# Kernel tuning notes

Hardware: AMD Instinct MI355X
Metric: run time of the kernel (lower is better)

## Reference

```python
import jax, jax.numpy as jnp
import numpy as np
from jax import lax

# Module hyperparameters (init_kwargs)
B, T, F, H = 512, 256, 64, 128
D = F + H            # decoder LSTMCell width = input_dim + hidden_rnn
OUT_DIM = 32         # output_dim (survival horizon steps)
RISKS = 2
NEG = -1e10


def lstm_cell(x, h, c, Wih, Whh):
    # PyTorch gate order: i, f, g, o; bias=False
    g = x @ Wih.T + h @ Whh.T
    i, f, gg, o = jnp.split(g, 4, axis=-1)
    c = jax.nn.sigmoid(f) * c + jax.nn.sigmoid(i) * jnp.tanh(gg)
    h = jax.nn.sigmoid(o) * jnp.tanh(c)
    return h, c


def setup_inputs() -> dict:
    key = jax.random.key(0)
    ks = jax.random.split(key, 12)
    rn = lambda k, shp, fan: jax.random.normal(k, shp, jnp.float32) * (1.0 / np.sqrt(fan))
    return {
        "x": jax.random.normal(ks[0], (B, T, F), jnp.float32),
        # encoder LSTM (1 layer, bias=False)
        "W_ih_emb": rn(ks[1], (4 * H, F), F),
        "W_hh_emb": rn(ks[2], (4 * H, H), H),
        # longitudinal head: Linear(H -> F)
        "W_long": rn(ks[3], (F, H), H),
        "b_long": jnp.zeros((F,), jnp.float32),
        # attention head: Linear(F+H -> 1)
        "W_att": rn(ks[4], (1, D), D),
        "b_att": jnp.zeros((1,), jnp.float32),
        # per-risk cause-specific LSTMCell (bias=False) and Linear(D -> 1)
        "W_ih_cs": rn(ks[5], (RISKS, 4 * D, D), D),
        "W_hh_cs": rn(ks[6], (RISKS, 4 * D, D), D),
        "W_cs": rn(ks[7], (RISKS, 1, D), D),
        "b_cs": jnp.zeros((RISKS, 1), jnp.float32),
    }


def _forward(x, W_ih_emb, W_hh_emb, W_long, b_long, W_att, b_att,
             W_ih_cs, W_hh_cs, W_cs, b_cs):
    inputmask = jnp.abs(x).sum(2) == 0                      # [B,T]
    last_obs = (~inputmask).sum(axis=1) - 1                 # [B]

    # encoder LSTM over time
    def enc_step(carry, xt):
        h, c = carry
        h, c = lstm_cell(xt, h, c, W_ih_emb, W_hh_emb)
        return (h, c), h

    h0 = jnp.zeros((x.shape[0], H), x.dtype)
    _, hs = lax.scan(enc_step, (h0, h0), x.transpose(1, 0, 2))
    hidden = hs.transpose(1, 0, 2)                          # [B,T,H]

    long_pred = hidden @ W_long.T + b_long                  # [B,T,F]

    x_last = x[jnp.arange(x.shape[0]), last_obs]            # [B,F]
    concat = jnp.concatenate(
        [hidden, jnp.broadcast_to(x_last[:, None, :], (x.shape[0], x.shape[1], F))], -1)
    scores = (concat @ W_att.T + b_att)[..., 0]             # [B,T]

    idx = jnp.arange(x.shape[1])[None, :]
    scores = jnp.where(idx >= last_obs[:, None], NEG, scores)
    att = jax.nn.softmax(scores, axis=1)
    att = jnp.where((last_obs > 0)[:, None], att, 0.0)      # rows with last_obs==0 zeroed

    hidden_att = jnp.einsum('bt,bth->bh', att, hidden)      # [B,H]
    ha = jnp.concatenate([hidden_att, x_last], 1)           # [B,D]

    state0 = (lax.stop_gradient(ha), lax.stop_gradient(ha))  # .detach() on init state
    rs = jnp.arange(OUT_DIM * RISKS) % RISKS                # k-major, r-minor loop order

    def dec_step(carry, r):
        h, c = carry
        h, c = lstm_cell(ha, h, c, W_ih_cs[r], W_hh_cs[r])
        out = jax.nn.sigmoid(h @ W_cs[r].T + b_cs[r])       # [B,1]
        return (h, c), out

    _, outs = lax.scan(dec_step, state0, rs)                # [steps,B,1]
    outcomes = jax.nn.softmax(outs[..., 0].T, axis=-1)      # [B, OUT_DIM*RISKS]
    parts = tuple(outcomes[:, i * OUT_DIM:(i + 1) * OUT_DIM] for i in range(RISKS))
    return (long_pred,) + parts


def reference(x, W_ih_emb, W_hh_emb, W_long, b_long, W_att, b_att,
              W_ih_cs, W_hh_cs, W_cs, b_cs):
    return _forward(x, W_ih_emb, W_hh_emb, W_long, b_long, W_att, b_att,
                    W_ih_cs, W_hh_cs, W_cs, b_cs)
```

## Files before the change

kernel.cpp:

```cpp
#include <hip/hip_runtime.h>
#include <stdint.h>

#define DEV __device__ __forceinline__
typedef unsigned short u16; typedef unsigned int u32; typedef unsigned long long u64;
typedef __attribute__((ext_vector_type(8))) short s8v;
typedef __attribute__((ext_vector_type(4))) float f4v;

#define Bb 512
#define Tt 256
#define Ff 64
#define Hh 128
#define Dd 192

DEV u16 f2bf(float f){ u32 u = __builtin_bit_cast(u32, f); u32 r = (u + 0x7fffu + ((u>>16)&1u)) >> 16; return (u16)r; }
DEV float bf2f(u16 h){ u32 u = ((u32)h)<<16; return __builtin_bit_cast(float, u); }
DEV float sigm(float x){ return __builtin_amdgcn_rcpf(1.0f + __expf(-x)); }
DEV float tanhfast(float x){ return 1.0f - 2.0f*__builtin_amdgcn_rcpf(1.0f + __expf(2.0f*x)); }

DEV f4v mfma16(s8v a, s8v b, f4v c){ return __builtin_amdgcn_mfma_f32_16x16x32_bf16(a, b, c, 0, 0, 0); }

DEV int hxe(int k, int c){ int blk = k>>3; return (blk*16 + (c ^ ((blk&3)<<1)))*8 + (k&7); }

DEV s8v pack8(const float* p){
  const float4 a = *(const float4*)p; const float4 b = *(const float4*)(p+4);
  s8v r; r[0]=(short)f2bf(a.x); r[1]=(short)f2bf(a.y); r[2]=(short)f2bf(a.z); r[3]=(short)f2bf(a.w);
  r[4]=(short)f2bf(b.x); r[5]=(short)f2bf(b.y); r[6]=(short)f2bf(b.z); r[7]=(short)f2bf(b.w); return r;
}

__global__ __launch_bounds__(64) void prelim_k(const float* __restrict__ x,
    const float* __restrict__ Watt, const float* __restrict__ batt,
    float* __restrict__ xlast, float* __restrict__ c0, int* __restrict__ lastobs)
{
  int b = blockIdx.x, tid = threadIdx.x;
  int cnt = 0;
  for (int it = 0; it < 4; ++it){
    int t = it*64 + tid;
    const float4* p = (const float4*)(x + ((size_t)b*Tt + t)*Ff);
    float s = 0.0f;
    #pragma unroll
    for (int q = 0; q < 16; ++q){ float4 v = p[q]; s += fabsf(v.x)+fabsf(v.y)+fabsf(v.z)+fabsf(v.w); }
    u64 m = __ballot(s != 0.0f);
    cnt += __popcll(m);
  }
  int last = cnt - 1;
  int li = (last < 0) ? (Tt-1) : last;
  float xl = x[((size_t)b*Tt + li)*Ff + tid];
  xlast[b*Ff + tid] = xl;
  float p = xl * Watt[Hh + tid];
  for (int off = 32; off; off >>= 1) p += __shfl_down(p, off);
  if (tid == 0){ c0[b] = p + batt[0]; lastobs[b] = last; }
}

__global__ __launch_bounds__(256) void prep_wd_k(const float* __restrict__ Whhcs, u16* __restrict__ Wd)
{
  int idx = blockIdx.x*256 + threadIdx.x;
  int j = idx & 7, l = (idx>>3)&63;
  int fidx = idx>>9;
  int kt = fidx % 6; int rem = fidx/6; int mt = rem & 3; rem >>= 2; int w = rem % 12; int r = rem/12;
  int gate = mt*Dd + w*16 + (l&15);
  int k = kt*32 + (l>>4)*8 + j;
  Wd[idx] = f2bf(Whhcs[((size_t)r*768 + gate)*Dd + k]);
}

__global__ __launch_bounds__(512) void enc_k(
    const float* __restrict__ x, const float* __restrict__ Whh, const float* __restrict__ Wih,
    const float* __restrict__ Wlong, const float* __restrict__ blong, const float* __restrict__ Watt,
    const float* __restrict__ xlast, const float* __restrict__ c0v, const int* __restrict__ lastobs,
    float* __restrict__ lp_out, float* __restrict__ ha)
{
  __shared__ __align__(16) u16 hx[3072];
  __shared__ float lp_lds[16*68];
  __shared__ float sarr[16];
  const int tid = threadIdx.x, wid = tid>>6, lane = tid&63, l15 = lane&15, l4 = lane>>4;
  const int b0 = blockIdx.x*16;
  const int xrow = tid>>5, xc2 = (tid&31)*2;

  s8v wf[4][6];
  #pragma unroll
  for (int mt = 0; mt < 4; ++mt){
    int gate = mt*Hh + wid*16 + l15;
    #pragma unroll
    for (int kt = 0; kt < 6; ++kt){
      int k0 = kt*32 + l4*8;
      if (kt < 4) wf[mt][kt] = pack8(Whh + (size_t)gate*Hh + k0);
      else        wf[mt][kt] = pack8(Wih + (size_t)gate*Ff + (k0 - Hh));
    }
  }
  s8v wfx[6];
  {
    s8v z = {0,0,0,0,0,0,0,0};
    #pragma unroll
    for (int kt = 0; kt < 6; ++kt) wfx[kt] = z;
    if (wid < 4){
      int f = wid*16 + l15;
      #pragma unroll
      for (int kt = 0; kt < 4; ++kt) wfx[kt] = pack8(Wlong + (size_t)f*Hh + kt*32 + l4*8);
    } else if (wid == 4 && l15 == 0){
      #pragma unroll
      for (int kt = 0; kt < 4; ++kt) wfx[kt] = pack8(Watt + kt*32 + l4*8);
    }
  }
  float bl[4] = {0,0,0,0};
  if (wid < 4){
    #pragma unroll
    for (int j = 0; j < 4; ++j) bl[j] = blong[wid*16 + l4*4 + j];
  }
  const int   lastb = lastobs[b0 + l15];
  const float c0b   = c0v[b0 + l15];

  ((u64*)hx)[tid] = 0ull;
  {
    float2 xv = *(const float2*)(x + ((size_t)(b0+xrow)*Tt + 0)*Ff + xc2);
    u32 pk = (u32)f2bf(xv.x) | ((u32)f2bf(xv.y)<<16);
    *(u32*)&hx[hxe(Hh + xc2, xrow)] = pk;
  }
  __syncthreads();

  float cst[4] = {0,0,0,0}, hval[4] = {0,0,0,0};
  float accA[4] = {0,0,0,0}, mrun = -3.0e38f, zrun = 0.0f;

  for (int t = 0; t < Tt; ++t){
    s8v bf[6];
    #pragma unroll
    for (int kt = 0; kt < 6; ++kt)
      bf[kt] = *(const s8v*)&hx[((kt*4 + l4)*16 + (l15 ^ (l4<<1)))*8];
    float2 xnext;
    if (t+1 < Tt) xnext = *(const float2*)(x + ((size_t)(b0+xrow)*Tt + (t+1))*Ff + xc2);

    f4v acc0 = {0,0,0,0}, acc1 = {0,0,0,0}, acc2 = {0,0,0,0}, acc3 = {0,0,0,0}, accx = {0,0,0,0};
    #pragma unroll
    for (int kt = 0; kt < 6; ++kt){
      acc0 = mfma16(wf[0][kt], bf[kt], acc0);
      acc1 = mfma16(wf[1][kt], bf[kt], acc1);
      acc2 = mfma16(wf[2][kt], bf[kt], acc2);
      acc3 = mfma16(wf[3][kt], bf[kt], acc3);
    }
    if (wid < 5){
      #pragma unroll
      for (int kt = 0; kt < 6; ++kt) accx = mfma16(wfx[kt], bf[kt], accx);
    }
    if (wid == 4 && l4 == 0) sarr[l15] = accx[0] + c0b;

    float hnew[4];
    #pragma unroll
    for (int j = 0; j < 4; ++j){
      float cn = sigm(acc1[j])*cst[j] + sigm(acc0[j])*tanhfast(acc2[j]);
      cst[j] = cn;
      hnew[j] = sigm(acc3[j])*tanhfast(cn);
    }
    __syncthreads();
    if (t >= 1){
      float s = sarr[l15];
      if (t-1 < lastb){
        float mn = fmaxf(mrun, s);
        float sc = __expf(mrun - mn);
        float e  = __expf(s - mn);
        zrun = zrun*sc + e;
        #pragma unroll
        for (int j = 0; j < 4; ++j) accA[j] = accA[j]*sc + e*hval[j];
        mrun = mn;
      }
    }
    #pragma unroll
    for (int j = 0; j < 4; ++j) hval[j] = hnew[j];
    #pragma unroll
    for (int j = 0; j < 4; ++j) hx[hxe(wid*16 + l4*4 + j, l15)] = (u16)f2bf(hnew[j]);
    if (t+1 < Tt){
      u32 pk = (u32)f2bf(xnext.x) | ((u32)f2bf(xnext.y)<<16);
      *(u32*)&hx[hxe(Hh + xc2, xrow)] = pk;
    }
    if (wid < 4){
      #pragma unroll
      for (int j = 0; j < 4; ++j)
        lp_lds[l15*68 + wid*16 + l4*4 + j] = accx[j] + bl[j];
    }
    __syncthreads();
    if (t >= 1){
      float2 v; v.x = lp_lds[xrow*68 + xc2]; v.y = lp_lds[xrow*68 + xc2 + 1];
      *(float2*)(lp_out + ((size_t)(b0+xrow)*Tt + (t-1))*Ff + xc2) = v;
    }
  }
  {
    s8v bf[4];
    #pragma unroll
    for (int kt = 0; kt < 4; ++kt)
      bf[kt] = *(const s8v*)&hx[((kt*4 + l4)*16 + (l15 ^ (l4<<1)))*8];
    if (wid < 4){
      f4v accx = {0,0,0,0};
      #pragma unroll
      for (int kt = 0; kt < 4; ++kt) accx = mfma16(wfx[kt], bf[kt], accx);
      #pragma unroll
      for (int j = 0; j < 4; ++j) lp_lds[l15*68 + wid*16 + l4*4 + j] = accx[j] + bl[j];
    }
    float inv = (zrun > 0.0f) ? __builtin_amdgcn_rcpf(zrun) : 0.0f;
    #pragma unroll
    for (int j = 0; j < 4; ++j)
      ha[(size_t)(b0 + l15)*Dd + wid*16 + l4*4 + j] = accA[j]*inv;
    __syncthreads();
    { float2 v; v.x = lp_lds[xrow*68 + xc2]; v.y = lp_lds[xrow*68 + xc2 + 1];
      *(float2*)(lp_out + ((size_t)(b0+xrow)*Tt + (Tt-1))*Ff + xc2) = v; }
    for (int q = tid; q < 16*Ff; q += 512){
      int r2 = q >> 6, f = q & 63;
      ha[(size_t)(b0 + r2)*Dd + Hh + f] = xlast[(b0 + r2)*Ff + f];
    }
  }
}

__global__ __launch_bounds__(768) void dec_k(const float* __restrict__ ha, const u16* __restrict__ Wd,
    const float* __restrict__ Wihcs, const float* __restrict__ Wcs, const float* __restrict__ bcs,
    float* __restrict__ outs)
{
  __shared__ __align__(16) u16 hx[3072];
  __shared__ float red[16*52];
  const int tid = threadIdx.x, wid = tid>>6, lane = tid&63, l15 = lane&15, l4 = lane>>4;
  const int b0 = blockIdx.x*16;
  {
    int k4 = tid>>4, c = tid&15, k = k4*4;
    float4 v = *(const float4*)(ha + (size_t)(b0+c)*Dd + k);
    int e = hxe(k, c);
    *(u32*)&hx[e]   = (u32)f2bf(v.x) | ((u32)f2bf(v.y)<<16);
    *(u32*)&hx[e+2] = (u32)f2bf(v.z) | ((u32)f2bf(v.w)<<16);
  }
  const int u0 = wid*16 + l4*4;
  float cst[4], wcs0[4], wcs1[4];
  #pragma unroll
  for (int j = 0; j < 4; ++j){
    cst[j]  = ha[(size_t)(b0+l15)*Dd + u0 + j];
    wcs0[j] = Wcs[u0 + j];
    wcs1[j] = Wcs[Dd + u0 + j];
  }
  const float bc0 = bcs[0], bc1 = bcs[1];
  __syncthreads();
  f4v xw0[4], xw1[4];
  {
    s8v haf[6];
    #pragma unroll
    for (int kt = 0; kt < 6; ++kt)
      haf[kt] = *(const s8v*)&hx[((kt*4 + l4)*16 + (l15 ^ (l4<<1)))*8];
    #pragma unroll
    for (int r = 0; r < 2; ++r)
      #pragma unroll
      for (int mt = 0; mt < 4; ++mt){
        f4v a = {0,0,0,0};
        #pragma unroll
        for (int kt = 0; kt < 6; ++kt){
          int gate = mt*Dd + wid*16 + l15;
          s8v w = pack8(Wihcs + ((size_t)r*768 + gate)*Dd + kt*32 + l4*8);
          a = mfma16(w, haf[kt], a);
        }
        if (r == 0) xw0[mt] = a; else xw1[mt] = a;
      }
  }
  for (int s = 0; s < 64; ++s){
    const int r = s & 1;
    s8v bf[6];
    #pragma unroll
    for (int kt = 0; kt < 6; ++kt)
      bf[kt] = *(const s8v*)&hx[((kt*4 + l4)*16 + (l15 ^ (l4<<1)))*8];
    const u16* wb = Wd + ((size_t)(r*12 + wid)*24)*512 + lane*8;
    f4v acc[4];
    s8v w0[6], w1[6];
    #pragma unroll
    for (int kt = 0; kt < 6; ++kt) w0[kt] = *(const s8v*)(wb + kt*512);
    {
      #pragma unroll
      for (int kt = 0; kt < 6; ++kt) w1[kt] = *(const s8v*)(wb + (6 + kt)*512);
      f4v a = r ? xw1[0] : xw0[0];
      #pragma unroll
      for (int kt = 0; kt < 6; ++kt) a = mfma16(w0[kt], bf[kt], a);
      acc[0] = a;
    }
    {
      #pragma unroll
      for (int kt = 0; kt < 6; ++kt) w0[kt] = *(const s8v*)(wb + (12 + kt)*512);
      f4v a = r ? xw1[1] : xw0[1];
      #pragma unroll
      for (int kt = 0; kt < 6; ++kt) a = mfma16(w1[kt], bf[kt], a);
      acc[1] = a;
    }
    {
      #pragma unroll
      for (int kt = 0; kt < 6; ++kt) w1[kt] = *(const s8v*)(wb + (18 + kt)*512);
      f4v a = r ? xw1[2] : xw0[2];
      #pragma unroll
      for (int kt = 0; kt < 6; ++kt) a = mfma16(w0[kt], bf[kt], a);
      acc[2] = a;
    }
    {
      f4v a = r ? xw1[3] : xw0[3];
      #pragma unroll
      for (int kt = 0; kt < 6; ++kt) a = mfma16(w1[kt], bf[kt], a);
      acc[3] = a;
    }
    float hnew[4], part = 0.0f;
    #pragma unroll
    for (int j = 0; j < 4; ++j){
      float cn = sigm(acc[1][j])*cst[j] + sigm(acc[0][j])*tanhfast(acc[2][j]);
      cst[j] = cn;
      hnew[j] = sigm(acc[3][j])*tanhfast(cn);
      part += hnew[j] * (r ? wcs1[j] : wcs0[j]);
    }
    __syncthreads();
    #pragma unroll
    for (int j = 0; j < 4; ++j) hx[hxe(u0 + j, l15)] = (u16)f2bf(hnew[j]);
    red[l15*52 + wid*4 + l4] = part;
    __syncthreads();
    if (tid < 16){
      float ssum = 0.0f;
      #pragma unroll
      for (int q = 0; q < 48; ++q) ssum += red[tid*52 + q];
      outs[s*Bb + b0 + tid] = sigm(ssum + (r ? bc1 : bc0));
    }
  }
}

__global__ __launch_bounds__(256) void fin_k(const float* __restrict__ outs, float* __restrict__ dout)
{
  int row = blockIdx.x*256 + threadIdx.x;
  float v[64]; float mx = -3.0e38f;
  #pragma unroll
  for (int s = 0; s < 64; ++s){ v[s] = outs[s*Bb + row]; mx = fmaxf(mx, v[s]); }
  float sum = 0.0f;
  #pragma unroll
  for (int s = 0; s < 64; ++s){ v[s] = __expf(v[s] - mx); sum += v[s]; }
  float inv = __builtin_amdgcn_rcpf(sum);
  float* p0 = dout + (size_t)Bb*Tt*Ff;
  float* p1 = p0 + Bb*32;
  #pragma unroll
  for (int j = 0; j < 32; ++j) p0[row*32 + j] = v[j]*inv;
  #pragma unroll
  for (int j = 0; j < 32; ++j) p1[row*32 + j] = v[32 + j]*inv;
}

extern "C" void kernel_launch(void* const* d_in, const int* in_sizes, int n_in,
                              void* d_out, int out_size, void* d_ws, size_t ws_size,
                              hipStream_t stream)
{
  const float* x      = (const float*)d_in[0];
  const float* Wih    = (const float*)d_in[1];
  const float* Whh    = (const float*)d_in[2];
  const float* Wlong  = (const float*)d_in[3];
  const float* blong  = (const float*)d_in[4];
  const float* Watt   = (const float*)d_in[5];
  const float* batt   = (const float*)d_in[6];
  const float* Wihcs  = (const float*)d_in[7];
  const float* Whhcs  = (const float*)d_in[8];
  const float* Wcs    = (const float*)d_in[9];
  const float* bcs    = (const float*)d_in[10];
  float* out = (float*)d_out;
  char* ws = (char*)d_ws;

  float* xlast   = (float*)ws;
  float* c0      = (float*)(ws + 131072);
  int*   lastobs = (int*)  (ws + 133120);
  float* ha      = (float*)(ws + 135168);
  u16*   Wd      = (u16*)  (ws + 528384);
  float* outs    = (float*)(ws + 1118208);

  prep_wd_k<<<1152, 256, 0, stream>>>(Whhcs, Wd);
  prelim_k<<<Bb, 64, 0, stream>>>(x, Watt, batt, xlast, c0, lastobs);
  enc_k<<<32, 512, 0, stream>>>(x, Whh, Wih, Wlong, blong, Watt, xlast, c0, lastobs, out, ha);
  dec_k<<<32, 768, 0, stream>>>(ha, Wd, Wihcs, Wcs, bcs, outs);
  fin_k<<<2, 256, 0, stream>>>(outs, out);
}
```

Baseline: 582.2 us.

## Double-buffer encoder LDS, precompute decoder input projections, register/LDS-resident decoder weights

```diff
diff --git a/kernel.cpp b/kernel.cpp
--- a/kernel.cpp
+++ b/kernel.cpp
@@ -26,6 +26,7 @@
   s8v r; r[0]=(short)f2bf(a.x); r[1]=(short)f2bf(a.y); r[2]=(short)f2bf(a.z); r[3]=(short)f2bf(a.w);
   r[4]=(short)f2bf(b.x); r[5]=(short)f2bf(b.y); r[6]=(short)f2bf(b.z); r[7]=(short)f2bf(b.w); return r;
 }
+DEV u32 pk2(float a, float b){ return (u32)f2bf(a) | ((u32)f2bf(b)<<16); }
 
 __global__ __launch_bounds__(64) void prelim_k(const float* __restrict__ x,
     const float* __restrict__ Watt, const float* __restrict__ batt,
@@ -51,26 +52,55 @@
   if (tid == 0){ c0[b] = p + batt[0]; lastobs[b] = last; }
 }
 
-__global__ __launch_bounds__(256) void prep_wd_k(const float* __restrict__ Whhcs, u16* __restrict__ Wd)
+__global__ __launch_bounds__(256) void prep_wd_k(const float* __restrict__ Whhcs,
+    const float* __restrict__ Wihcs, u16* __restrict__ Wd, u16* __restrict__ WdIH)
 {
   int idx = blockIdx.x*256 + threadIdx.x;
-  int j = idx & 7, l = (idx>>3)&63;
-  int fidx = idx>>9;
-  int kt = fidx % 6; int rem = fidx/6; int mt = rem & 3; rem >>= 2; int w = rem % 12; int r = rem/12;
-  int gate = mt*Dd + w*16 + (l&15);
-  int k = kt*32 + (l>>4)*8 + j;
-  Wd[idx] = f2bf(Whhcs[((size_t)r*768 + gate)*Dd + k]);
-}
-
-__global__ __launch_bounds__(512) void enc_k(
+  int j = idx & 7, lane = (idx>>3)&63;
+  int f = idx>>9;
+  int kt = f % 6; int mtr = f/6;
+  int mt = mtr % 48, r = mtr/48;
+  int ut = mt>>2, g = mt&3;
+  int row = g*Dd + ut*16 + (lane&15);
+  int k = kt*32 + (lane>>4)*8 + j;
+  size_t src = ((size_t)r*768 + row)*Dd + k;
+  Wd[idx]   = f2bf(Whhcs[src]);
+  WdIH[idx] = f2bf(Wihcs[src]);
+}
+
+__global__ __launch_bounds__(64) void xw_k(const u16* __restrict__ WdIH,
+    const float* __restrict__ ha, u16* __restrict__ xwg)
+{
+  int lane = threadIdx.x, l15 = lane&15, l4 = lane>>4;
+  int cg = blockIdx.x & 3, rm = blockIdx.x >> 2;
+  s8v af[6];
+  #pragma unroll
+  for (int kt=0;kt<6;++kt) af[kt] = *(const s8v*)(WdIH + (size_t)(rm*6+kt)*512 + lane*8);
+  #pragma unroll
+  for (int ct=0; ct<8; ++ct){
+    int c = cg*128 + ct*16 + l15;
+    f4v a = {0,0,0,0};
+    #pragma unroll
+    for (int kt=0;kt<6;++kt){
+      s8v b = pack8(ha + (size_t)c*Dd + kt*32 + l4*8);
+      a = mfma16(af[kt], b, a);
+    }
+    int bg = cg*8 + ct;
+    int base = bg*24576 + rm*256 + l15*16 + l4*4;
+    *(u32*)&xwg[base]   = pk2(a[0], a[1]);
+    *(u32*)&xwg[base+2] = pk2(a[2], a[3]);
+  }
+}
+
+__global__ __launch_bounds__(512,2) void enc_k(
     const float* __restrict__ x, const float* __restrict__ Whh, const float* __restrict__ Wih,
     const float* __restrict__ Wlong, const float* __restrict__ blong, const float* __restrict__ Watt,
     const float* __restrict__ xlast, const float* __restrict__ c0v, const int* __restrict__ lastobs,
     float* __restrict__ lp_out, float* __restrict__ ha)
 {
-  __shared__ __align__(16) u16 hx[3072];
-  __shared__ float lp_lds[16*68];
-  __shared__ float sarr[16];
+  __shared__ __align__(16) u16 hx[2][3072];
+  __shared__ float lp_lds[2][16*68];
+  __shared__ float sarr[2][16];
   const int tid = threadIdx.x, wid = tid>>6, lane = tid&63, l15 = lane&15, l4 = lane>>4;
   const int b0 = blockIdx.x*16;
   const int xrow = tid>>5, xc2 = (tid&31)*2;
@@ -108,97 +138,123 @@
   const int   lastb = lastobs[b0 + l15];
   const float c0b   = c0v[b0 + l15];
 
-  ((u64*)hx)[tid] = 0ull;
+  const int he0 = hxe(wid*16 + l4*4, l15);
+  const int xe0 = hxe(Hh + xc2, xrow);
+
+  ((u64*)hx[0])[tid] = 0ull;
   {
     float2 xv = *(const float2*)(x + ((size_t)(b0+xrow)*Tt + 0)*Ff + xc2);
-    u32 pk = (u32)f2bf(xv.x) | ((u32)f2bf(xv.y)<<16);
-    *(u32*)&hx[hxe(Hh + xc2, xrow)] = pk;
-  }
+    *(u32*)&hx[0][xe0] = pk2(xv.x, xv.y);
+  }
+  float2 xa[4], xb[4];
+  #pragma unroll
+  for (int u = 0; u < 4; ++u)
+    xa[u] = *(const float2*)(x + ((size_t)(b0+xrow)*Tt + (1+u))*Ff + xc2);
   __syncthreads();
 
-  float cst[4] = {0,0,0,0}, hval[4] = {0,0,0,0};
+  float cst[4] = {0,0,0,0}, hp[4] = {0,0,0,0}, hpp[4] = {0,0,0,0};
   float accA[4] = {0,0,0,0}, mrun = -3.0e38f, zrun = 0.0f;
 
-  for (int t = 0; t < Tt; ++t){
-    s8v bf[6];
-    #pragma unroll
-    for (int kt = 0; kt < 6; ++kt)
-      bf[kt] = *(const s8v*)&hx[((kt*4 + l4)*16 + (l15 ^ (l4<<1)))*8];
-    float2 xnext;
-    if (t+1 < Tt) xnext = *(const float2*)(x + ((size_t)(b0+xrow)*Tt + (t+1))*Ff + xc2);
-
-    f4v acc0 = {0,0,0,0}, acc1 = {0,0,0,0}, acc2 = {0,0,0,0}, acc3 = {0,0,0,0}, accx = {0,0,0,0};
-    #pragma unroll
-    for (int kt = 0; kt < 6; ++kt){
-      acc0 = mfma16(wf[0][kt], bf[kt], acc0);
-      acc1 = mfma16(wf[1][kt], bf[kt], acc1);
-      acc2 = mfma16(wf[2][kt], bf[kt], acc2);
-      acc3 = mfma16(wf[3][kt], bf[kt], acc3);
-    }
-    if (wid < 5){
-      #pragma unroll
-      for (int kt = 0; kt < 6; ++kt) accx = mfma16(wfx[kt], bf[kt], accx);
-    }
-    if (wid == 4 && l4 == 0) sarr[l15] = accx[0] + c0b;
-
-    float hnew[4];
-    #pragma unroll
-    for (int j = 0; j < 4; ++j){
-      float cn = sigm(acc1[j])*cst[j] + sigm(acc0[j])*tanhfast(acc2[j]);
-      cst[j] = cn;
-      hnew[j] = sigm(acc3[j])*tanhfast(cn);
-    }
-    __syncthreads();
-    if (t >= 1){
-      float s = sarr[l15];
-      if (t-1 < lastb){
-        float mn = fmaxf(mrun, s);
-        float sc = __expf(mrun - mn);
-        float e  = __expf(s - mn);
-        zrun = zrun*sc + e;
+  for (int tb = 0; tb < Tt; tb += 4){
+    #pragma unroll
+    for (int u = 0; u < 4; ++u){
+      int tp = tb + 5 + u; if (tp > Tt-1) tp = Tt-1;
+      xb[u] = *(const float2*)(x + ((size_t)(b0+xrow)*Tt + tp)*Ff + xc2);
+    }
+    #pragma unroll
+    for (int u = 0; u < 4; ++u){
+      const int t = tb + u;
+      const int curb = u & 1, nxtb = curb ^ 1;
+      s8v bf[6];
+      #pragma unroll
+      for (int kt = 0; kt < 6; ++kt)
+        bf[kt] = *(const s8v*)&hx[curb][((kt*4 + l4)*16 + (l15 ^ (l4<<1)))*8];
+
+      f4v acc0 = {0,0,0,0}, acc1 = {0,0,0,0}, acc2 = {0,0,0,0}, acc3 = {0,0,0,0}, accx = {0,0,0,0};
+      #pragma unroll
+      for (int kt = 0; kt < 6; ++kt){
+        acc0 = mfma16(wf[0][kt], bf[kt], acc0);
+        acc1 = mfma16(wf[1][kt], bf[kt], acc1);
+        acc2 = mfma16(wf[2][kt], bf[kt], acc2);
+        acc3 = mfma16(wf[3][kt], bf[kt], acc3);
+      }
+      if (wid < 5){
         #pragma unroll
-        for (int j = 0; j < 4; ++j) accA[j] = accA[j]*sc + e*hval[j];
-        mrun = mn;
-      }
-    }
-    #pragma unroll
-    for (int j = 0; j < 4; ++j) hval[j] = hnew[j];
-    #pragma unroll
-    for (int j = 0; j < 4; ++j) hx[hxe(wid*16 + l4*4 + j, l15)] = (u16)f2bf(hnew[j]);
-    if (t+1 < Tt){
-      u32 pk = (u32)f2bf(xnext.x) | ((u32)f2bf(xnext.y)<<16);
-      *(u32*)&hx[hxe(Hh + xc2, xrow)] = pk;
-    }
-    if (wid < 4){
-      #pragma unroll
-      for (int j = 0; j < 4; ++j)
-        lp_lds[l15*68 + wid*16 + l4*4 + j] = accx[j] + bl[j];
-    }
-    __syncthreads();
-    if (t >= 1){
-      float2 v; v.x = lp_lds[xrow*68 + xc2]; v.y = lp_lds[xrow*68 + xc2 + 1];
-      *(float2*)(lp_out + ((size_t)(b0+xrow)*Tt + (t-1))*Ff + xc2) = v;
-    }
+        for (int kt = 0; kt < 6; ++kt) accx = mfma16(wfx[kt], bf[kt], accx);
+      }
+      if (wid == 4 && l4 == 0) sarr[nxtb][l15] = accx[0] + c0b;
+
+      float hnew[4];
+      #pragma unroll
+      for (int j = 0; j < 4; ++j){
+        float cn = sigm(acc1[j])*cst[j] + sigm(acc0[j])*tanhfast(acc2[j]);
+        cst[j] = cn;
+        hnew[j] = sigm(acc3[j])*tanhfast(cn);
+      }
+      if (t >= 2){
+        float sv = sarr[curb][l15];
+        if (t-2 < lastb){
+          float mn = fmaxf(mrun, sv);
+          float sc = __expf(mrun - mn);
+          float e  = __expf(sv - mn);
+          zrun = zrun*sc + e;
+          #pragma unroll
+          for (int j = 0; j < 4; ++j) accA[j] = accA[j]*sc + e*hpp[j];
+          mrun = mn;
+        }
+      }
+      #pragma unroll
+      for (int j = 0; j < 4; ++j){ hpp[j] = hp[j]; hp[j] = hnew[j]; }
+      {
+        u64 w = (u64)pk2(hnew[0],hnew[1]) | ((u64)pk2(hnew[2],hnew[3])<<32);
+        *(u64*)&hx[nxtb][he0] = w;
+      }
+      if (t < Tt-1) *(u32*)&hx[nxtb][xe0] = pk2(xa[u].x, xa[u].y);
+      if (wid < 4){
+        #pragma unroll
+        for (int j = 0; j < 4; ++j)
+          lp_lds[nxtb][l15*68 + wid*16 + l4*4 + j] = accx[j] + bl[j];
+      }
+      if (t >= 2){
+        float2 v; v.x = lp_lds[curb][xrow*68 + xc2]; v.y = lp_lds[curb][xrow*68 + xc2 + 1];
+        *(float2*)(lp_out + ((size_t)(b0+xrow)*Tt + (t-2))*Ff + xc2) = v;
+      }
+      __syncthreads();
+    }
+    #pragma unroll
+    for (int u = 0; u < 4; ++u) xa[u] = xb[u];
   }
   {
-    s8v bf[4];
+    if (254 < lastb){
+      float sv = sarr[0][l15];
+      float mn = fmaxf(mrun, sv);
+      float sc = __expf(mrun - mn);
+      float e  = __expf(sv - mn);
+      zrun = zrun*sc + e;
+      #pragma unroll
+      for (int j = 0; j < 4; ++j) accA[j] = accA[j]*sc + e*hpp[j];
+      mrun = mn;
+    }
+    { float2 v; v.x = lp_lds[0][xrow*68 + xc2]; v.y = lp_lds[0][xrow*68 + xc2 + 1];
+      *(float2*)(lp_out + ((size_t)(b0+xrow)*Tt + 254)*Ff + xc2) = v; }
+    s8v bfE[4];
     #pragma unroll
     for (int kt = 0; kt < 4; ++kt)
-      bf[kt] = *(const s8v*)&hx[((kt*4 + l4)*16 + (l15 ^ (l4<<1)))*8];
+      bfE[kt] = *(const s8v*)&hx[0][((kt*4 + l4)*16 + (l15 ^ (l4<<1)))*8];
     if (wid < 4){
       f4v accx = {0,0,0,0};
       #pragma unroll
-      for (int kt = 0; kt < 4; ++kt) accx = mfma16(wfx[kt], bf[kt], accx);
-      #pragma unroll
-      for (int j = 0; j < 4; ++j) lp_lds[l15*68 + wid*16 + l4*4 + j] = accx[j] + bl[j];
+      for (int kt = 0; kt < 4; ++kt) accx = mfma16(wfx[kt], bfE[kt], accx);
+      #pragma unroll
+      for (int j = 0; j < 4; ++j) lp_lds[1][l15*68 + wid*16 + l4*4 + j] = accx[j] + bl[j];
     }
     float inv = (zrun > 0.0f) ? __builtin_amdgcn_rcpf(zrun) : 0.0f;
     #pragma unroll
     for (int j = 0; j < 4; ++j)
       ha[(size_t)(b0 + l15)*Dd + wid*16 + l4*4 + j] = accA[j]*inv;
     __syncthreads();
-    { float2 v; v.x = lp_lds[xrow*68 + xc2]; v.y = lp_lds[xrow*68 + xc2 + 1];
-      *(float2*)(lp_out + ((size_t)(b0+xrow)*Tt + (Tt-1))*Ff + xc2) = v; }
+    { float2 v; v.x = lp_lds[1][xrow*68 + xc2]; v.y = lp_lds[1][xrow*68 + xc2 + 1];
+      *(float2*)(lp_out + ((size_t)(b0+xrow)*Tt + 255)*Ff + xc2) = v; }
     for (int q = tid; q < 16*Ff; q += 512){
       int r2 = q >> 6, f = q & 63;
       ha[(size_t)(b0 + r2)*Dd + Hh + f] = xlast[(b0 + r2)*Ff + f];
@@ -206,112 +262,155 @@
   }
 }
 
-__global__ __launch_bounds__(768) void dec_k(const float* __restrict__ ha, const u16* __restrict__ Wd,
-    const float* __restrict__ Wihcs, const float* __restrict__ Wcs, const float* __restrict__ bcs,
-    float* __restrict__ outs)
-{
-  __shared__ __align__(16) u16 hx[3072];
-  __shared__ float red[16*52];
+__global__ __launch_bounds__(256,1) void dec_k(const float* __restrict__ ha,
+    const u16* __restrict__ Wd, const u16* __restrict__ xwg,
+    const float* __restrict__ Wcs, const float* __restrict__ bcs, float* __restrict__ outs)
+{
+  __shared__ __align__(16) u16 hx[2][3072];
+  __shared__ __align__(16) u16 w1[48*2*512];
+  __shared__ __align__(16) u16 xwl[2*48*256];
+  __shared__ float red[2][4][16];
   const int tid = threadIdx.x, wid = tid>>6, lane = tid&63, l15 = lane&15, l4 = lane>>4;
   const int b0 = blockIdx.x*16;
-  {
-    int k4 = tid>>4, c = tid&15, k = k4*4;
+
+  #pragma unroll
+  for (int it = 0; it < 3; ++it){
+    int k = it*64 + (tid>>4)*4, c = tid&15;
     float4 v = *(const float4*)(ha + (size_t)(b0+c)*Dd + k);
     int e = hxe(k, c);
-    *(u32*)&hx[e]   = (u32)f2bf(v.x) | ((u32)f2bf(v.y)<<16);
-    *(u32*)&hx[e+2] = (u32)f2bf(v.z) | ((u32)f2bf(v.w)<<16);
-  }
-  const int u0 = wid*16 + l4*4;
-  float cst[4], wcs0[4], wcs1[4];
-  #pragma unroll
-  for (int j = 0; j < 4; ++j){
-    cst[j]  = ha[(size_t)(b0+l15)*Dd + u0 + j];
-    wcs0[j] = Wcs[u0 + j];
-    wcs1[j] = Wcs[Dd + u0 + j];
+    *(u32*)&hx[0][e]   = pk2(v.x, v.y);
+    *(u32*)&hx[0][e+2] = pk2(v.z, v.w);
+  }
+  {
+    const u16* src = xwg + (size_t)blockIdx.x*24576;
+    #pragma unroll
+    for (int i = 0; i < 12; ++i){
+      int off = (i*256 + tid)*8;
+      *(s8v*)&xwl[off] = *(const s8v*)(src + off);
+    }
+  }
+  #pragma unroll
+  for (int i = 0; i < 24; ++i){
+    int off = (i*256 + tid)*8;
+    int chunk = off>>9, inner = off&511;
+    int mtg = chunk>>1, kt = chunk&1;
+    *(s8v*)&w1[off] = *(const s8v*)(Wd + (size_t)((48+mtg)*6+kt)*512 + inner);
+  }
+  s8v wreg[12][6];
+  #pragma unroll
+  for (int m = 0; m < 12; ++m)
+    #pragma unroll
+    for (int kt = 0; kt < 6; ++kt)
+      wreg[m][kt] = *(const s8v*)(Wd + (size_t)((wid*12+m)*6+kt)*512 + lane*8);
+
+  float cst[3][4], wcsr0[3][4], wcsr1[3][4];
+  #pragma unroll
+  for (int ut = 0; ut < 3; ++ut){
+    int u0 = (wid*3+ut)*16 + l4*4;
+    #pragma unroll
+    for (int jj = 0; jj < 4; ++jj){
+      cst[ut][jj]   = ha[(size_t)(b0+l15)*Dd + u0 + jj];
+      wcsr0[ut][jj] = Wcs[u0 + jj];
+      wcsr1[ut][jj] = Wcs[Dd + u0 + jj];
+    }
   }
   const float bc0 = bcs[0], bc1 = bcs[1];
   __syncthreads();
-  f4v xw0[4], xw1[4];
-  {
-    s8v haf[6];
-    #pragma unroll
-    for (int kt = 0; kt < 6; ++kt)
-      haf[kt] = *(const s8v*)&hx[((kt*4 + l4)*16 + (l15 ^ (l4<<1)))*8];
-    #pragma unroll
-    for (int r = 0; r < 2; ++r)
-      #pragma unroll
-      for (int mt = 0; mt < 4; ++mt){
-        f4v a = {0,0,0,0};
+
+  const u16* wsb = Wd + (size_t)(48 + wid*12)*6*512 + lane*8;
+  s8v lA[4], lB[4];
+#define LOADA(m) { _Pragma("unroll") for (int q=0;q<4;++q) lA[q] = *(const s8v*)(wsb + (size_t)((m)*6 + 2 + q)*512); }
+#define LOADB(m) { _Pragma("unroll") for (int q=0;q<4;++q) lB[q] = *(const s8v*)(wsb + (size_t)((m)*6 + 2 + q)*512); }
+
+#define XWINIT(r_, m_, a_) { \
+    int xb_ = ((r_)*48 + wid*12 + (m_))*256 + l15*16 + l4*4; \
+    u32 q0 = *(const u32*)&xwl[xb_]; u32 q1 = *(const u32*)&xwl[xb_+2]; \
+    a_[0] = bf2f((u16)q0); a_[1] = bf2f((u16)(q0>>16)); \
+    a_[2] = bf2f((u16)q1); a_[3] = bf2f((u16)(q1>>16)); }
+
+#define CELLS(r_, ut_, wcs_, a0_, a1_, a2_, a3_) { \
+    float hn0,hn1,hn2,hn3; \
+    { float cn = sigm(a1_[0])*cst[ut_][0] + sigm(a0_[0])*tanhfast(a2_[0]); cst[ut_][0]=cn; hn0 = sigm(a3_[0])*tanhfast(cn); } \
+    { float cn = sigm(a1_[1])*cst[ut_][1] + sigm(a0_[1])*tanhfast(a2_[1]); cst[ut_][1]=cn; hn1 = sigm(a3_[1])*tanhfast(cn); } \
+    { float cn = sigm(a1_[2])*cst[ut_][2] + sigm(a0_[2])*tanhfast(a2_[2]); cst[ut_][2]=cn; hn2 = sigm(a3_[2])*tanhfast(cn); } \
+    { float cn = sigm(a1_[3])*cst[ut_][3] + sigm(a0_[3])*tanhfast(a2_[3]); cst[ut_][3]=cn; hn3 = sigm(a3_[3])*tanhfast(cn); } \
+    part += hn0*wcs_[ut_][0] + hn1*wcs_[ut_][1] + hn2*wcs_[ut_][2] + hn3*wcs_[ut_][3]; \
+    int u0_ = (wid*3+(ut_))*16 + l4*4; \
+    int e0_ = (((u0_>>3)*16) + (l15 ^ (((u0_>>3)&3)<<1)))*8 + (u0_&7); \
+    u64 w_ = (u64)pk2(hn0,hn1) | ((u64)pk2(hn2,hn3)<<32); \
+    *(u64*)&hx[nxtb_][e0_] = w_; }
+
+  for (int sp = 0; sp < 32; ++sp){
+    {
+      LOADA(0); LOADB(1);
+      const int nxtb_ = 1;
+      s8v bf[6];
+      #pragma unroll
+      for (int kt = 0; kt < 6; ++kt)
+        bf[kt] = *(const s8v*)&hx[0][((kt*4 + l4)*16 + (l15 ^ (l4<<1)))*8];
+      float part = 0.0f;
+      #pragma unroll
+      for (int ut = 0; ut < 3; ++ut){
+        f4v a0,a1,a2,a3;
+        XWINIT(0, ut*4+0, a0); XWINIT(0, ut*4+1, a1); XWINIT(0, ut*4+2, a2); XWINIT(0, ut*4+3, a3);
         #pragma unroll
         for (int kt = 0; kt < 6; ++kt){
-          int gate = mt*Dd + wid*16 + l15;
-          s8v w = pack8(Wihcs + ((size_t)r*768 + gate)*Dd + kt*32 + l4*8);
-          a = mfma16(w, haf[kt], a);
+          a0 = mfma16(wreg[ut*4+0][kt], bf[kt], a0);
+          a1 = mfma16(wreg[ut*4+1][kt], bf[kt], a1);
+          a2 = mfma16(wreg[ut*4+2][kt], bf[kt], a2);
+          a3 = mfma16(wreg[ut*4+3][kt], bf[kt], a3);
         }
-        if (r == 0) xw0[mt] = a; else xw1[mt] = a;
-      }
-  }
-  for (int s = 0; s < 64; ++s){
-    const int r = s & 1;
-    s8v bf[6];
-    #pragma unroll
-    for (int kt = 0; kt < 6; ++kt)
-      bf[kt] = *(const s8v*)&hx[((kt*4 + l4)*16 + (l15 ^ (l4<<1)))*8];
-    const u16* wb = Wd + ((size_t)(r*12 + wid)*24)*512 + lane*8;
-    f4v acc[4];
-    s8v w0[6], w1[6];
-    #pragma unroll
-    for (int kt = 0; kt < 6; ++kt) w0[kt] = *(const s8v*)(wb + kt*512);
+        CELLS(0, ut, wcsr0, a0, a1, a2, a3);
+      }
+      part += __shfl_xor(part, 16); part += __shfl_xor(part, 32);
+      if (l4 == 0) red[0][wid][l15] = part;
+      __syncthreads();
+      if (tid < 16)
+        outs[(sp*2)*Bb + b0 + tid] = sigm(red[0][0][tid]+red[0][1][tid]+red[0][2][tid]+red[0][3][tid] + bc0);
+    }
     {
-      #pragma unroll
-      for (int kt = 0; kt < 6; ++kt) w1[kt] = *(const s8v*)(wb + (6 + kt)*512);
-      f4v a = r ? xw1[0] : xw0[0];
-      #pragma unroll
-      for (int kt = 0; kt < 6; ++kt) a = mfma16(w0[kt], bf[kt], a);
-      acc[0] = a;
-    }
-    {
-      #pragma unroll
-      for (int kt = 0; kt < 6; ++kt) w0[kt] = *(const s8v*)(wb + (12 + kt)*512);
-      f4v a = r ? xw1[1] : xw0[1];
-      #pragma unroll
-      for (int kt = 0; kt < 6; ++kt) a = mfma16(w1[kt], bf[kt], a);
-      acc[1] = a;
-    }
-    {
-      #pragma unroll
-      for (int kt = 0; kt < 6; ++kt) w1[kt] = *(const s8v*)(wb + (18 + kt)*512);
-      f4v a = r ? xw1[2] : xw0[2];
-      #pragma unroll
-      for (int kt = 0; kt < 6; ++kt) a = mfma16(w0[kt], bf[kt], a);
-      acc[2] = a;
-    }
-    {
-      f4v a = r ? xw1[3] : xw0[3];
-      #pragma unroll
-      for (int kt = 0; kt < 6; ++kt) a = mfma16(w1[kt], bf[kt], a);
-      acc[3] = a;
-    }
-    float hnew[4], part = 0.0f;
-    #pragma unroll
-    for (int j = 0; j < 4; ++j){
-      float cn = sigm(acc[1][j])*cst[j] + sigm(acc[0][j])*tanhfast(acc[2][j]);
-      cst[j] = cn;
-      hnew[j] = sigm(acc[3][j])*tanhfast(cn);
-      part += hnew[j] * (r ? wcs1[j] : wcs0[j]);
-    }
-    __syncthreads();
-    #pragma unroll
-    for (int j = 0; j < 4; ++j) hx[hxe(u0 + j, l15)] = (u16)f2bf(hnew[j]);
-    red[l15*52 + wid*4 + l4] = part;
-    __syncthreads();
-    if (tid < 16){
-      float ssum = 0.0f;
-      #pragma unroll
-      for (int q = 0; q < 48; ++q) ssum += red[tid*52 + q];
-      outs[s*Bb + b0 + tid] = sigm(ssum + (r ? bc1 : bc0));
-    }
-  }
+      const int nxtb_ = 0;
+      s8v bf[6];
+      #pragma unroll
+      for (int kt = 0; kt < 6; ++kt)
+        bf[kt] = *(const s8v*)&hx[1][((kt*4 + l4)*16 + (l15 ^ (l4<<1)))*8];
+      float part = 0.0f;
+      #pragma unroll
+      for (int ut = 0; ut < 3; ++ut){
+        f4v a0,a1,a2,a3;
+        XWINIT(1, ut*4+0, a0); XWINIT(1, ut*4+1, a1); XWINIT(1, ut*4+2, a2); XWINIT(1, ut*4+3, a3);
+        #pragma unroll
+        for (int g = 0; g < 4; ++g){
+          const int m = ut*4 + g;
+          f4v* ap = (g==0)? &a0 : (g==1)? &a1 : (g==2)? &a2 : &a3;
+          f4v a = *ap;
+          { s8v w0 = *(const s8v*)&w1[((wid*12+m)*2+0)*512 + lane*8];
+            s8v w1v= *(const s8v*)&w1[((wid*12+m)*2+1)*512 + lane*8];
+            a = mfma16(w0, bf[0], a); a = mfma16(w1v, bf[1], a); }
+          if ((m&1)==0){
+            a = mfma16(lA[0], bf[2], a); a = mfma16(lA[1], bf[3], a);
+            a = mfma16(lA[2], bf[4], a); a = mfma16(lA[3], bf[5], a);
+            if (m+2 < 12) LOADA(m+2);
+          } else {
+            a = mfma16(lB[0], bf[2], a); a = mfma16(lB[1], bf[3], a);
+            a = mfma16(lB[2], bf[4], a); a = mfma16(lB[3], bf[5], a);
+            if (m+2 < 12) LOADB(m+2);
+          }
+          *ap = a;
+        }
+        CELLS(1, ut, wcsr1, a0, a1, a2, a3);
+      }
+      part += __shfl_xor(part, 16); part += __shfl_xor(part, 32);
+      if (l4 == 0) red[1][wid][l15] = part;
+      __syncthreads();
+      if (tid < 16)
+        outs[(sp*2+1)*Bb + b0 + tid] = sigm(red[1][0][tid]+red[1][1][tid]+red[1][2][tid]+red[1][3][tid] + bc1);
+    }
+  }
+#undef LOADA
+#undef LOADB
+#undef XWINIT
+#undef CELLS
 }
 
 __global__ __launch_bounds__(256) void fin_k(const float* __restrict__ outs, float* __restrict__ dout)
@@ -355,11 +454,14 @@
   int*   lastobs = (int*)  (ws + 133120);
   float* ha      = (float*)(ws + 135168);
   u16*   Wd      = (u16*)  (ws + 528384);
-  float* outs    = (float*)(ws + 1118208);
-
-  prep_wd_k<<<1152, 256, 0, stream>>>(Whhcs, Wd);
+  u16*   WdIH    = (u16*)  (ws + 1118208);
+  u16*   xwg     = (u16*)  (ws + 1708032);
+  float* outs    = (float*)(ws + 3280896);
+
+  prep_wd_k<<<1152, 256, 0, stream>>>(Whhcs, Wihcs, Wd, WdIH);
   prelim_k<<<Bb, 64, 0, stream>>>(x, Watt, batt, xlast, c0, lastobs);
   enc_k<<<32, 512, 0, stream>>>(x, Whh, Wih, Wlong, blong, Watt, xlast, c0, lastobs, out, ha);
-  dec_k<<<32, 768, 0, stream>>>(ha, Wd, Wihcs, Wcs, bcs, outs);
+  xw_k<<<384, 64, 0, stream>>>(WdIH, ha, xwg);
+  dec_k<<<32, 256, 0, stream>>>(ha, Wd, xwg, Wcs, bcs, outs);
   fin_k<<<2, 256, 0, stream>>>(outs, out);
 }
```

Measured after the change: 619.2 us. 1.06x slower.
